# Kernel optimization log

Measured on AMD Instinct MI355X. Metric: run time of the kernel, lower is better.

The kernel has to match this reference:

```python
import jax, jax.numpy as jnp
import numpy as np

EPS = 1e-5  # torch BatchNorm2d default eps


def setup_inputs() -> dict:
    key = jax.random.key(0)
    ks = jax.random.split(key, 11)
    n, c, h, w = 16, 512, 64, 64
    grp, cg, mip = 4, 128, 16
    return {
        "x": jax.random.normal(ks[0], (n, c, h, w), dtype=jnp.float32),
        "W1": jax.random.normal(ks[1], (mip, cg), dtype=jnp.float32) * 0.05,
        "b1": jax.random.normal(ks[2], (mip,), dtype=jnp.float32) * 0.05,
        "gamma": jax.random.uniform(ks[3], (mip,), dtype=jnp.float32, minval=0.5, maxval=1.5),
        "beta": jax.random.normal(ks[4], (mip,), dtype=jnp.float32) * 0.05,
        "mean": jax.random.normal(ks[5], (mip,), dtype=jnp.float32) * 0.05,
        "var": jax.random.uniform(ks[6], (mip,), dtype=jnp.float32, minval=0.5, maxval=1.5),
        "Wh": jax.random.normal(ks[7], (cg, mip), dtype=jnp.float32) * 0.1,
        "bh": jax.random.normal(ks[8], (cg,), dtype=jnp.float32) * 0.05,
        "Ww": jax.random.normal(ks[9], (cg, mip), dtype=jnp.float32) * 0.1,
        "bw": jax.random.normal(ks[10], (cg,), dtype=jnp.float32) * 0.05,
    }


def reference(x, W1, b1, gamma, beta, mean, var, Wh, bh, Ww, bw):
    n, c, h, w = x.shape
    grp = 4
    cg = c // grp
    # Since c % 4 == 0, torch.split gives 4 equal groups: fold group into a new axis.
    xg = x.reshape(n, grp, cg, h, w)                       # (n,g,cg,h,w)
    gh = xg.mean(axis=4)                                   # pool over w -> (n,g,cg,h)
    gw = xg.mean(axis=3)                                   # pool over h -> (n,g,cg,w)
    y = jnp.concatenate([gh, gw], axis=3)                  # (n,g,cg,h+w)
    # conv1 (1x1) shared across all 4 groups
    y = jnp.einsum('ngcl,mc->ngml', y, W1) + b1[None, None, :, None]
    # BatchNorm2d (eval mode, running stats)
    scale = gamma / jnp.sqrt(var + EPS)
    y = y * scale[None, None, :, None] + (beta - mean * scale)[None, None, :, None]
    # h_swish: x * relu6(x+3)/6
    y = y * (jnp.clip(y + 3.0, 0.0, 6.0) / 6.0)
    yh, yw = y[..., :h], y[..., h:]                        # (n,g,mip,h), (n,g,mip,w)
    a_h = jax.nn.sigmoid(jnp.einsum('ngml,cm->ngcl', yh, Wh) + bh[None, None, :, None])
    a_w = jax.nn.sigmoid(jnp.einsum('ngml,cm->ngcl', yw, Ww) + bw[None, None, :, None])
    out = xg * a_h[..., :, None] * a_w[..., None, :]       # (n,g,cg,h,w)
    out = out.reshape(n, c, h, w)
    # channel shuffle: (n, cg, grp, h, w) -> permute group axis forward
    out = out.reshape(n, cg, grp, h, w).transpose(0, 2, 1, 3, 4).reshape(n, c, h, w)
    return out
```

## Files before the change

### kernel.cpp

```cpp
#include <hip/hip_runtime.h>

#define N_   16
#define C_   512
#define GRP  4
#define CG   128
#define MIP  16

__device__ __forceinline__ float bf_lo(unsigned u) { return __uint_as_float(u << 16); }
__device__ __forceinline__ float bf_hi(unsigned u) { return __uint_as_float(u & 0xFFFF0000u); }
__device__ __forceinline__ float bf1(unsigned short s) { return __uint_as_float((unsigned)s << 16); }

__device__ __forceinline__ float ld_scalar(const void* p, int i, bool isbf) {
    return isbf ? bf1(((const unsigned short*)p)[i]) : ((const float*)p)[i];
}

__device__ __forceinline__ bool wave_sniff_isbf(const unsigned* __restrict__ x32,
                                                int lane) {
    int cnt = 0;
    #pragma unroll
    for (int k = 0; k < 4; ++k) {
        unsigned w = x32[lane + 64 * k];
        unsigned e = (w >> 7) & 0xFFu;
        cnt += (e >= 0x60u && e <= 0x9Fu) ? 1 : 0;
    }
    #pragma unroll
    for (int off = 32; off > 0; off >>= 1) cnt += __shfl_xor(cnt, off, 64);
    return cnt >= 192;
}

__device__ __forceinline__ bool sniff_isbf(const unsigned* __restrict__ x32,
                                           int t, unsigned* s_flag) {
    if (t < 64) {
        int cnt = 0;
        #pragma unroll
        for (int k = 0; k < 4; ++k) {
            unsigned w = x32[t + 64 * k];
            unsigned e = (w >> 7) & 0xFFu;
            cnt += (e >= 0x60u && e <= 0x9Fu) ? 1 : 0;
        }
        #pragma unroll
        for (int off = 32; off > 0; off >>= 1) cnt += __shfl_down(cnt, off, 64);
        if (t == 0) *s_flag = (cnt >= 192) ? 1u : 0u;
    }
    __syncthreads();
    return *s_flag != 0u;
}

__global__ __launch_bounds__(256) void kreduce(const void* __restrict__ xv,
                                               float* __restrict__ gh,
                                               float* __restrict__ gw) {
    const int lane = threadIdx.x & 63;
    const int tile = blockIdx.x * 4 + (threadIdx.x >> 6);
    const bool isbf = wave_sniff_isbf((const unsigned*)xv, lane);

    if (isbf) {
        const uint4* src = (const uint4*)((const unsigned short*)xv + (size_t)tile * 4096);
        float cp[8] = {0,0,0,0,0,0,0,0};
        #pragma unroll
        for (int i = 0; i < 8; ++i) {
            uint4 v = src[i * 64 + lane];
            unsigned uu[4] = {v.x, v.y, v.z, v.w};
            float rp = 0.f;
            #pragma unroll
            for (int k = 0; k < 4; ++k) {
                float f0 = bf_lo(uu[k]), f1 = bf_hi(uu[k]);
                rp += f0 + f1;
                cp[2*k] += f0; cp[2*k+1] += f1;
            }
            rp += __shfl_xor(rp, 1, 64);
            rp += __shfl_xor(rp, 2, 64);
            rp += __shfl_xor(rp, 4, 64);
            if ((lane & 7) == 0)
                gh[(size_t)tile * 64 + i * 8 + (lane >> 3)] = rp * (1.f/64.f);
        }
        #pragma unroll
        for (int k = 0; k < 8; ++k) {
            cp[k] += __shfl_xor(cp[k], 8, 64);
            cp[k] += __shfl_xor(cp[k], 16, 64);
            cp[k] += __shfl_xor(cp[k], 32, 64);
        }
        if (lane < 8) {
            float4 a = make_float4(cp[0]*(1.f/64.f), cp[1]*(1.f/64.f),
                                   cp[2]*(1.f/64.f), cp[3]*(1.f/64.f));
            float4 b = make_float4(cp[4]*(1.f/64.f), cp[5]*(1.f/64.f),
                                   cp[6]*(1.f/64.f), cp[7]*(1.f/64.f));
            float4* dst = (float4*)(gw + (size_t)tile * 64 + lane * 8);
            dst[0] = a; dst[1] = b;
        }
    } else {
        const float4* src = (const float4*)((const float*)xv + (size_t)tile * 4096);
        float cp[4] = {0,0,0,0};
        #pragma unroll
        for (int i = 0; i < 16; ++i) {
            float4 v = src[i * 64 + lane];
            float rp = (v.x + v.y) + (v.z + v.w);
            cp[0] += v.x; cp[1] += v.y; cp[2] += v.z; cp[3] += v.w;
            rp += __shfl_xor(rp, 1, 64);
            rp += __shfl_xor(rp, 2, 64);
            rp += __shfl_xor(rp, 4, 64);
            rp += __shfl_xor(rp, 8, 64);
            if ((lane & 15) == 0)
                gh[(size_t)tile * 64 + i * 4 + (lane >> 4)] = rp * (1.f/64.f);
        }
        #pragma unroll
        for (int k = 0; k < 4; ++k) {
            cp[k] += __shfl_xor(cp[k], 16, 64);
            cp[k] += __shfl_xor(cp[k], 32, 64);
        }
        if (lane < 16) {
            float4 a = make_float4(cp[0]*(1.f/64.f), cp[1]*(1.f/64.f),
                                   cp[2]*(1.f/64.f), cp[3]*(1.f/64.f));
            *(float4*)(gw + (size_t)tile * 64 + lane * 4) = a;
        }
    }
}

__global__ __launch_bounds__(256) void ky(
    const void* __restrict__ xv,
    const float* __restrict__ gh, const float* __restrict__ gw,
    const void* __restrict__ W1, const void* __restrict__ b1,
    const void* __restrict__ gamma, const void* __restrict__ beta,
    const void* __restrict__ mean, const void* __restrict__ var,
    float* __restrict__ y)
{
    __shared__ float W1_s[MIP * CG];
    __shared__ float scale_s[MIP], shift_s[MIP], b1_s[MIP];
    __shared__ unsigned flag_s;

    const int t = threadIdx.x;
    const bool isbf = sniff_isbf((const unsigned*)xv, t, &flag_s);

    if (isbf) {
        uint4 v = ((const uint4*)W1)[t];
        unsigned uu[4] = {v.x, v.y, v.z, v.w};
        #pragma unroll
        for (int k = 0; k < 4; ++k) {
            W1_s[t * 8 + 2 * k]     = bf_lo(uu[k]);
            W1_s[t * 8 + 2 * k + 1] = bf_hi(uu[k]);
        }
    } else {
        #pragma unroll
        for (int it = 0; it < 2; ++it) {
            int idx = t + 256 * it;
            float4 v = ((const float4*)W1)[idx];
            W1_s[idx * 4]     = v.x;
            W1_s[idx * 4 + 1] = v.y;
            W1_s[idx * 4 + 2] = v.z;
            W1_s[idx * 4 + 3] = v.w;
        }
    }
    if (t < MIP) {
        float sc = ld_scalar(gamma, t, isbf) * rsqrtf(ld_scalar(var, t, isbf) + 1e-5f);
        scale_s[t] = sc;
        shift_s[t] = ld_scalar(beta, t, isbf) - ld_scalar(mean, t, isbf) * sc;
        b1_s[t] = ld_scalar(b1, t, isbf);
    }
    __syncthreads();

    const int l = t & 127;
    const int half = t >> 7;
    const size_t base = (size_t)blockIdx.x * (CG * 64);
    const float* src = (l < 64) ? (gh + base + l) : (gw + base + (l - 64));
    float acc[8] = {0.f, 0.f, 0.f, 0.f, 0.f, 0.f, 0.f, 0.f};
    for (int cc = 0; cc < CG; ++cc) {
        float v = src[(size_t)cc * 64];
        #pragma unroll
        for (int mm = 0; mm < 8; ++mm)
            acc[mm] += W1_s[(half * 8 + mm) * CG + cc] * v;
    }
    float* yb = y + (size_t)blockIdx.x * (MIP * 128);
    #pragma unroll
    for (int mm = 0; mm < 8; ++mm) {
        int m = half * 8 + mm;
        float yv = acc[mm] + b1_s[m];
        yv = yv * scale_s[m] + shift_s[m];
        float hc = fminf(fmaxf(yv + 3.0f, 0.0f), 6.0f);
        yb[m * 128 + l] = yv * hc * (1.0f / 6.0f);
    }
}

__global__ __launch_bounds__(256) void kapply(const void* __restrict__ xv,
                                              const float* __restrict__ y,
                                              const void* __restrict__ Wh,
                                              const void* __restrict__ bh,
                                              const void* __restrict__ Ww,
                                              const void* __restrict__ bw,
                                              void* __restrict__ outv) {
    const int lane = threadIdx.x & 63;
    const int bid = blockIdx.x * 4 + (threadIdx.x >> 6);
    const bool isbf = wave_sniff_isbf((const unsigned*)xv, lane);

    const int n = bid >> 9;
    const int o = bid & 511;
    const int p = (o & 127) * 4 + (o >> 7);
    const int g = p >> 7, cc = p & 127;

    const float* ysrc = y + (size_t)(n * 4 + g) * (MIP * 128);
    float acch = ld_scalar(bh, cc, isbf);
    float accw = ld_scalar(bw, cc, isbf);
    #pragma unroll
    for (int m = 0; m < MIP; ++m) {
        float wh = ld_scalar(Wh, cc * MIP + m, isbf);
        float ww = ld_scalar(Ww, cc * MIP + m, isbf);
        acch += wh * ysrc[m * 128 + lane];
        accw += ww * ysrc[m * 128 + 64 + lane];
    }
    const float ah_r = 1.0f / (1.0f + __expf(-acch));
    const float aw_r = 1.0f / (1.0f + __expf(-accw));

    if (isbf) {
        float awv[8];
        #pragma unroll
        for (int k = 0; k < 8; ++k)
            awv[k] = __shfl(aw_r, (lane & 7) * 8 + k, 64);
        const uint4* src = (const uint4*)((const unsigned short*)xv + ((size_t)n * 512 + p) * 4096);
        uint4* dst = (uint4*)((unsigned short*)outv + (size_t)bid * 4096);
        #pragma unroll
        for (int i = 0; i < 8; ++i) {
            float sah = __shfl(ah_r, i * 8 + (lane >> 3), 64);
            uint4 v = src[i * 64 + lane];
            unsigned uu[4] = {v.x, v.y, v.z, v.w};
            unsigned res[4];
            #pragma unroll
            for (int k = 0; k < 4; ++k) {
                float f0 = bf_lo(uu[k]) * sah * awv[2*k];
                float f1 = bf_hi(uu[k]) * sah * awv[2*k+1];
                unsigned u0 = __float_as_uint(f0); u0 += 0x7FFFu + ((u0 >> 16) & 1u);
                unsigned u1 = __float_as_uint(f1); u1 += 0x7FFFu + ((u1 >> 16) & 1u);
                res[k] = (u0 >> 16) | (u1 & 0xFFFF0000u);
            }
            uint4 w2; w2.x = res[0]; w2.y = res[1]; w2.z = res[2]; w2.w = res[3];
            dst[i * 64 + lane] = w2;
        }
    } else {
        float awv[4];
        #pragma unroll
        for (int k = 0; k < 4; ++k)
            awv[k] = __shfl(aw_r, (lane & 15) * 4 + k, 64);
        const float4* src = (const float4*)((const float*)xv + ((size_t)n * 512 + p) * 4096);
        float4* dst = (float4*)((float*)outv + (size_t)bid * 4096);
        #pragma unroll
        for (int i = 0; i < 16; ++i) {
            float sah = __shfl(ah_r, i * 4 + (lane >> 4), 64);
            float4 v = src[i * 64 + lane];
            v.x *= sah * awv[0];
            v.y *= sah * awv[1];
            v.z *= sah * awv[2];
            v.w *= sah * awv[3];
            dst[i * 64 + lane] = v;
        }
    }
}

extern "C" void kernel_launch(void* const* d_in, const int* in_sizes, int n_in,
                              void* d_out, int out_size, void* d_ws, size_t ws_size,
                              hipStream_t stream) {
    const void* x     = d_in[0];
    const void* W1    = d_in[1];
    const void* b1    = d_in[2];
    const void* gamma = d_in[3];
    const void* beta  = d_in[4];
    const void* mean  = d_in[5];
    const void* var   = d_in[6];
    const void* Wh    = d_in[7];
    const void* bh    = d_in[8];
    const void* Ww    = d_in[9];
    const void* bw    = d_in[10];

    float* ws = (float*)d_ws;
    float* gh = ws;
    float* gw = gh + 524288;
    float* yv = gw + 524288;

    kreduce<<<2048, 256, 0, stream>>>(x, gh, gw);
    ky<<<N_ * GRP, 256, 0, stream>>>(x, gh, gw, W1, b1, gamma, beta, mean, var, yv);
    kapply<<<2048, 256, 0, stream>>>(x, yv, Wh, bh, Ww, bw, d_out);
}
```

Baseline: 286.4 us.

## Fuse squeeze-excite MLP into apply kernel, recomputing y per block

Merges the small y-computation kernel into the apply kernel: each block recomputes the conv1+BN+h_swish result for its (batch, group) into shared memory, then applies attention to 8 output channels. This removes a low-parallelism 64-block launch and the global round trip for y. It adds redundant per-block recomputation and an extra barrier before the streaming phase, and halves the block count of the apply stage.

```diff
diff --git a/kernel.cpp b/kernel.cpp
--- a/kernel.cpp
+++ b/kernel.cpp
@@ -26,24 +26,6 @@
     #pragma unroll
     for (int off = 32; off > 0; off >>= 1) cnt += __shfl_xor(cnt, off, 64);
     return cnt >= 192;
-}
-
-__device__ __forceinline__ bool sniff_isbf(const unsigned* __restrict__ x32,
-                                           int t, unsigned* s_flag) {
-    if (t < 64) {
-        int cnt = 0;
-        #pragma unroll
-        for (int k = 0; k < 4; ++k) {
-            unsigned w = x32[t + 64 * k];
-            unsigned e = (w >> 7) & 0xFFu;
-            cnt += (e >= 0x60u && e <= 0x9Fu) ? 1 : 0;
-        }
-        #pragma unroll
-        for (int off = 32; off > 0; off >>= 1) cnt += __shfl_down(cnt, off, 64);
-        if (t == 0) *s_flag = (cnt >= 192) ? 1u : 0u;
-    }
-    __syncthreads();
-    return *s_flag != 0u;
 }
 
 __global__ __launch_bounds__(256) void kreduce(const void* __restrict__ xv,
@@ -115,20 +97,25 @@
     }
 }
 
-__global__ __launch_bounds__(256) void ky(
+__global__ __launch_bounds__(256) void kfused(
     const void* __restrict__ xv,
     const float* __restrict__ gh, const float* __restrict__ gw,
     const void* __restrict__ W1, const void* __restrict__ b1,
     const void* __restrict__ gamma, const void* __restrict__ beta,
     const void* __restrict__ mean, const void* __restrict__ var,
-    float* __restrict__ y)
+    const void* __restrict__ Wh, const void* __restrict__ bh,
+    const void* __restrict__ Ww, const void* __restrict__ bw,
+    void* __restrict__ outv)
 {
     __shared__ float W1_s[MIP * CG];
+    __shared__ float y_s[MIP * 128];
     __shared__ float scale_s[MIP], shift_s[MIP], b1_s[MIP];
-    __shared__ unsigned flag_s;
 
     const int t = threadIdx.x;
-    const bool isbf = sniff_isbf((const unsigned*)xv, t, &flag_s);
+    const int lane = t & 63;
+    const int wv = t >> 6;
+    const int b = blockIdx.x;
+    const bool isbf = wave_sniff_isbf((const unsigned*)xv, lane);
 
     if (isbf) {
         uint4 v = ((const uint4*)W1)[t];
@@ -157,97 +144,94 @@
     }
     __syncthreads();
 
-    const int l = t & 127;
-    const int half = t >> 7;
-    const size_t base = (size_t)blockIdx.x * (CG * 64);
-    const float* src = (l < 64) ? (gh + base + l) : (gw + base + (l - 64));
-    float acc[8] = {0.f, 0.f, 0.f, 0.f, 0.f, 0.f, 0.f, 0.f};
-    for (int cc = 0; cc < CG; ++cc) {
-        float v = src[(size_t)cc * 64];
-        #pragma unroll
-        for (int mm = 0; mm < 8; ++mm)
-            acc[mm] += W1_s[(half * 8 + mm) * CG + cc] * v;
-    }
-    float* yb = y + (size_t)blockIdx.x * (MIP * 128);
+    const int n  = b >> 6;
+    const int o0 = (8 * b) & 511;
+    const int p0 = (o0 & 127) * 4 + (o0 >> 7);
+    const int g  = p0 >> 7;
+    const size_t base = (size_t)(n * 4 + g) * 8192;
+
+    {
+        const int l = t & 127;
+        const int half = t >> 7;
+        const float* src = (l < 64) ? (gh + base + l) : (gw + base + (l - 64));
+        float acc[8] = {0.f, 0.f, 0.f, 0.f, 0.f, 0.f, 0.f, 0.f};
+        for (int cc = 0; cc < CG; ++cc) {
+            float v = src[(size_t)cc * 64];
+            #pragma unroll
+            for (int mm = 0; mm < 8; ++mm)
+                acc[mm] += W1_s[(half * 8 + mm) * CG + cc] * v;
+        }
+        #pragma unroll
+        for (int mm = 0; mm < 8; ++mm) {
+            int m = half * 8 + mm;
+            float yv = acc[mm] + b1_s[m];
+            yv = yv * scale_s[m] + shift_s[m];
+            float hc = fminf(fmaxf(yv + 3.0f, 0.0f), 6.0f);
+            y_s[m * 128 + l] = yv * hc * (1.0f / 6.0f);
+        }
+    }
+    __syncthreads();
+
     #pragma unroll
-    for (int mm = 0; mm < 8; ++mm) {
-        int m = half * 8 + mm;
-        float yv = acc[mm] + b1_s[m];
-        yv = yv * scale_s[m] + shift_s[m];
-        float hc = fminf(fmaxf(yv + 3.0f, 0.0f), 6.0f);
-        yb[m * 128 + l] = yv * hc * (1.0f / 6.0f);
-    }
-}
-
-__global__ __launch_bounds__(256) void kapply(const void* __restrict__ xv,
-                                              const float* __restrict__ y,
-                                              const void* __restrict__ Wh,
-                                              const void* __restrict__ bh,
-                                              const void* __restrict__ Ww,
-                                              const void* __restrict__ bw,
-                                              void* __restrict__ outv) {
-    const int lane = threadIdx.x & 63;
-    const int bid = blockIdx.x * 4 + (threadIdx.x >> 6);
-    const bool isbf = wave_sniff_isbf((const unsigned*)xv, lane);
-
-    const int n = bid >> 9;
-    const int o = bid & 511;
-    const int p = (o & 127) * 4 + (o >> 7);
-    const int g = p >> 7, cc = p & 127;
-
-    const float* ysrc = y + (size_t)(n * 4 + g) * (MIP * 128);
-    float acch = ld_scalar(bh, cc, isbf);
-    float accw = ld_scalar(bw, cc, isbf);
-    #pragma unroll
-    for (int m = 0; m < MIP; ++m) {
-        float wh = ld_scalar(Wh, cc * MIP + m, isbf);
-        float ww = ld_scalar(Ww, cc * MIP + m, isbf);
-        acch += wh * ysrc[m * 128 + lane];
-        accw += ww * ysrc[m * 128 + 64 + lane];
-    }
-    const float ah_r = 1.0f / (1.0f + __expf(-acch));
-    const float aw_r = 1.0f / (1.0f + __expf(-accw));
-
-    if (isbf) {
-        float awv[8];
-        #pragma unroll
-        for (int k = 0; k < 8; ++k)
-            awv[k] = __shfl(aw_r, (lane & 7) * 8 + k, 64);
-        const uint4* src = (const uint4*)((const unsigned short*)xv + ((size_t)n * 512 + p) * 4096);
-        uint4* dst = (uint4*)((unsigned short*)outv + (size_t)bid * 4096);
-        #pragma unroll
-        for (int i = 0; i < 8; ++i) {
-            float sah = __shfl(ah_r, i * 8 + (lane >> 3), 64);
-            uint4 v = src[i * 64 + lane];
-            unsigned uu[4] = {v.x, v.y, v.z, v.w};
-            unsigned res[4];
-            #pragma unroll
-            for (int k = 0; k < 4; ++k) {
-                float f0 = bf_lo(uu[k]) * sah * awv[2*k];
-                float f1 = bf_hi(uu[k]) * sah * awv[2*k+1];
-                unsigned u0 = __float_as_uint(f0); u0 += 0x7FFFu + ((u0 >> 16) & 1u);
-                unsigned u1 = __float_as_uint(f1); u1 += 0x7FFFu + ((u1 >> 16) & 1u);
-                res[k] = (u0 >> 16) | (u1 & 0xFFFF0000u);
+    for (int j = 0; j < 2; ++j) {
+        const int bid = 8 * b + wv * 2 + j;
+        const int o = bid & 511;
+        const int p = (o & 127) * 4 + (o >> 7);
+        const int cc = p & 127;
+
+        float acch = ld_scalar(bh, cc, isbf);
+        float accw = ld_scalar(bw, cc, isbf);
+        #pragma unroll
+        for (int m = 0; m < MIP; ++m) {
+            float wh = ld_scalar(Wh, cc * MIP + m, isbf);
+            float ww = ld_scalar(Ww, cc * MIP + m, isbf);
+            acch += wh * y_s[m * 128 + lane];
+            accw += ww * y_s[m * 128 + 64 + lane];
+        }
+        const float ah_r = 1.0f / (1.0f + __expf(-acch));
+        const float aw_r = 1.0f / (1.0f + __expf(-accw));
+
+        if (isbf) {
+            float awv[8];
+            #pragma unroll
+            for (int k = 0; k < 8; ++k)
+                awv[k] = __shfl(aw_r, (lane & 7) * 8 + k, 64);
+            const uint4* src = (const uint4*)((const unsigned short*)xv + ((size_t)n * 512 + p) * 4096);
+            uint4* dst = (uint4*)((unsigned short*)outv + (size_t)bid * 4096);
+            #pragma unroll
+            for (int i = 0; i < 8; ++i) {
+                float sah = __shfl(ah_r, i * 8 + (lane >> 3), 64);
+                uint4 v = src[i * 64 + lane];
+                unsigned uu[4] = {v.x, v.y, v.z, v.w};
+                unsigned res[4];
+                #pragma unroll
+                for (int k = 0; k < 4; ++k) {
+                    float f0 = bf_lo(uu[k]) * sah * awv[2*k];
+                    float f1 = bf_hi(uu[k]) * sah * awv[2*k+1];
+                    unsigned u0 = __float_as_uint(f0); u0 += 0x7FFFu + ((u0 >> 16) & 1u);
+                    unsigned u1 = __float_as_uint(f1); u1 += 0x7FFFu + ((u1 >> 16) & 1u);
+                    res[k] = (u0 >> 16) | (u1 & 0xFFFF0000u);
+                }
+                uint4 w2; w2.x = res[0]; w2.y = res[1]; w2.z = res[2]; w2.w = res[3];
+                dst[i * 64 + lane] = w2;
             }
-            uint4 w2; w2.x = res[0]; w2.y = res[1]; w2.z = res[2]; w2.w = res[3];
-            dst[i * 64 + lane] = w2;
-        }
-    } else {
-        float awv[4];
-        #pragma unroll
-        for (int k = 0; k < 4; ++k)
-            awv[k] = __shfl(aw_r, (lane & 15) * 4 + k, 64);
-        const float4* src = (const float4*)((const float*)xv + ((size_t)n * 512 + p) * 4096);
-        float4* dst = (float4*)((float*)outv + (size_t)bid * 4096);
-        #pragma unroll
-        for (int i = 0; i < 16; ++i) {
-            float sah = __shfl(ah_r, i * 4 + (lane >> 4), 64);
-            float4 v = src[i * 64 + lane];
-            v.x *= sah * awv[0];
-            v.y *= sah * awv[1];
-            v.z *= sah * awv[2];
-            v.w *= sah * awv[3];
-            dst[i * 64 + lane] = v;
+        } else {
+            float awv[4];
+            #pragma unroll
+            for (int k = 0; k < 4; ++k)
+                awv[k] = __shfl(aw_r, (lane & 15) * 4 + k, 64);
+            const float4* src = (const float4*)((const float*)xv + ((size_t)n * 512 + p) * 4096);
+            float4* dst = (float4*)((float*)outv + (size_t)bid * 4096);
+            #pragma unroll
+            for (int i = 0; i < 16; ++i) {
+                float sah = __shfl(ah_r, i * 4 + (lane >> 4), 64);
+                float4 v = src[i * 64 + lane];
+                v.x *= sah * awv[0];
+                v.y *= sah * awv[1];
+                v.z *= sah * awv[2];
+                v.w *= sah * awv[3];
+                dst[i * 64 + lane] = v;
+            }
         }
     }
 }
@@ -270,9 +254,8 @@
     float* ws = (float*)d_ws;
     float* gh = ws;
     float* gw = gh + 524288;
-    float* yv = gw + 524288;
 
     kreduce<<<2048, 256, 0, stream>>>(x, gh, gw);
-    ky<<<N_ * GRP, 256, 0, stream>>>(x, gh, gw, W1, b1, gamma, beta, mean, var, yv);
-    kapply<<<2048, 256, 0, stream>>>(x, yv, Wh, bh, Ww, bw, d_out);
-}
+    kfused<<<1024, 256, 0, stream>>>(x, gh, gw, W1, b1, gamma, beta, mean, var,
+                                     Wh, bh, Ww, bw, d_out);
+}
```

Measured after the change: 286.3 us. No clear change (-0.0%).
